# Performance work log

Measured on AMD Instinct MI355X. Metric: run time of the kernel, lower is better.

## Reference

```python
import jax, jax.numpy as jnp
import numpy as np
import math

NUM_HEAD = 16
D_MODEL = 1024
BATCH = 2
SEQ = 2048


def setup_inputs() -> dict:
    key = jax.random.key(0)
    k1, k2, k3, k4 = jax.random.split(key, 4)
    scale = 1.0 / math.sqrt(D_MODEL)
    return {
        "query": jax.random.normal(k1, (BATCH, SEQ, D_MODEL), dtype=jnp.float32),
        "key": jax.random.normal(k2, (BATCH, SEQ, D_MODEL), dtype=jnp.float32),
        "value": jax.random.normal(k3, (BATCH, SEQ, D_MODEL), dtype=jnp.float32),
        "w_concat": jax.random.normal(k4, (D_MODEL, D_MODEL), dtype=jnp.float32) * scale,
    }


def _split_heads(x):
    # [B, S, D] -> [B, H, S, d_k]
    B, S, D = x.shape
    return x.reshape(B, S, NUM_HEAD, D // NUM_HEAD).transpose(0, 2, 1, 3)


def reference(query, key, value, w_concat):
    # NOTE: faithful to the source bug — the w_q/w_k/w_v projections are
    # computed then discarded in the original forward; attention runs on the
    # raw (split) inputs.
    q = _split_heads(query)
    k = _split_heads(key)
    v = _split_heads(value)
    d_k = q.shape[-1]
    scores = jnp.einsum("bhqd,bhkd->bhqk", q, k) / math.sqrt(d_k)
    attn = jax.nn.softmax(scores, axis=-1)
    ctx = jnp.einsum("bhqk,bhkd->bhqd", attn, v)
    B, H, S, dk = ctx.shape
    x = ctx.transpose(0, 2, 1, 3).reshape(B, S, H * dk)
    # torch Linear (bias=False): y = x @ W^T
    return x @ w_concat.T
```

## Files before the change

### kernel.cpp

```cpp
#include <hip/hip_runtime.h>

#define BB 2
#define HH 16
#define SS 2048
#define DMODEL 1024

typedef unsigned short ushort_t;
typedef short bf16x8 __attribute__((ext_vector_type(8)));
typedef float f32x4 __attribute__((ext_vector_type(4)));

__device__ __forceinline__ unsigned short f2bf(float f) {
  union { float f; unsigned int u; } x; x.f = f;
  unsigned int u = x.u;
  return (unsigned short)((u + 0x7fffu + ((u >> 16) & 1u)) >> 16);
}
__device__ __forceinline__ unsigned int pack2(float a, float b) {
  return (unsigned int)f2bf(a) | ((unsigned int)f2bf(b) << 16);
}
__device__ __forceinline__ unsigned int cvtpk(float lo, float hi) {
  unsigned int r;
  asm("v_cvt_pk_bf16_f32 %0, %1, %2" : "=v"(r) : "v"(lo), "v"(hi));
  return r;
}
__device__ __forceinline__ void gload16(const ushort_t* g, ushort_t* l) {
  __builtin_amdgcn_global_load_lds(
      (const __attribute__((address_space(1))) void*)g,
      (__attribute__((address_space(3))) void*)l, 16, 0, 0);
}

__global__ void __launch_bounds__(256)
conv_qkv(const float* __restrict__ q, const float* __restrict__ k,
         const float* __restrict__ v, ushort_t* __restrict__ Qh,
         ushort_t* __restrict__ Kh, ushort_t* __restrict__ Vt) {
  const float c_sc = 0.18033688011112042f;
  __shared__ float vlds[64][65];
  int bh = blockIdx.y;
  int b = bh >> 4, h = bh & 15;
  int s0 = blockIdx.x * 64;
  int t = threadIdx.x;
#pragma unroll
  for (int j = 0; j < 4; ++j) {
    int idx = t + j * 256;
    int r = idx >> 4, c4 = idx & 15;
    size_t in_off = ((size_t)(b * SS + s0 + r)) * DMODEL + h * 64 + c4 * 4;
    float4 qa = *(const float4*)(q + in_off);
    float4 ka = *(const float4*)(k + in_off);
    float4 va = *(const float4*)(v + in_off);
    size_t out_off = ((size_t)bh * SS + s0 + r) * 64 + c4 * 4;
    *(uint2*)(Qh + out_off) = make_uint2(pack2(qa.x * c_sc, qa.y * c_sc),
                                         pack2(qa.z * c_sc, qa.w * c_sc));
    *(uint2*)(Kh + out_off) = make_uint2(pack2(ka.x, ka.y), pack2(ka.z, ka.w));
    vlds[r][c4 * 4 + 0] = va.x;
    vlds[r][c4 * 4 + 1] = va.y;
    vlds[r][c4 * 4 + 2] = va.z;
    vlds[r][c4 * 4 + 3] = va.w;
  }
  __syncthreads();
#pragma unroll
  for (int j = 0; j < 4; ++j) {
    int idx = t + j * 256;
    int d = idx >> 4, u = idx & 15;
    int c = ((u >> 3) << 1) | (u & 1);
    int g = (u >> 1) & 3;
    int m0 = c * 16 + g * 4;
    size_t voff = ((size_t)bh * 64 + d) * SS + s0 + u * 4;
    *(uint2*)(Vt + voff) =
        make_uint2(pack2(vlds[m0 + 0][d], vlds[m0 + 1][d]),
                   pack2(vlds[m0 + 2][d], vlds[m0 + 3][d]));
  }
}

__global__ void __launch_bounds__(256)
conv_w(const float* __restrict__ w, ushort_t* __restrict__ wb) {
  int i = blockIdx.x * 256 + threadIdx.x;
  float4 a = *(const float4*)(w + (size_t)i * 8);
  float4 b = *(const float4*)(w + (size_t)i * 8 + 4);
  uint4 o;
  o.x = pack2(a.x, a.y);
  o.y = pack2(a.z, a.w);
  o.z = pack2(b.x, b.y);
  o.w = pack2(b.z, b.w);
  *(uint4*)(wb + (size_t)i * 8) = o;
}

__global__ void __launch_bounds__(512, 1)
attn_fwd(const ushort_t* __restrict__ Qh, const ushort_t* __restrict__ Kh,
         const ushort_t* __restrict__ Vt, ushort_t* __restrict__ ctx) {
  __shared__ ushort_t K_lds[2][2][64][64];
  __shared__ ushort_t V_lds[2][2][64][64];
  __shared__ float cmb[4][64][21];
  int bh = blockIdx.y;
  int q0 = blockIdx.x * 256;
  int tid = threadIdx.x;
  int wid = tid >> 6;
  int half = wid >> 2;
  int wq = wid & 3;
  int lane = tid & 63;
  int g = lane >> 4, lr = lane & 15;
  int rsub = lane >> 3, ch = (lane & 7) ^ rsub;

  const ushort_t* Qp = Qh + (size_t)bh * SS * 64;
  const ushort_t* Kp = Kh + (size_t)bh * SS * 64;
  const ushort_t* Vp = Vt + (size_t)bh * 64 * SS;

  ushort_t (*Kl)[64][64] = K_lds[half];
  ushort_t (*Vl)[64][64] = V_lds[half];
  const int kvbase = half * (SS / 2);

  bf16x8 qf[4][2];
#pragma unroll
  for (int qb = 0; qb < 4; ++qb) {
    int row = q0 + wq * 64 + qb * 16 + lr;
#pragma unroll
    for (int kk = 0; kk < 2; ++kk)
      qf[qb][kk] = *(const bf16x8*)(Qp + (size_t)row * 64 + kk * 32 + g * 8);
  }

  const f32x4 vzero = {0.f, 0.f, 0.f, 0.f};
  const short ob = (short)0x3F80;
  const bf16x8 ones = {ob, ob, ob, ob, ob, ob, ob, ob};
  f32x4 o[4][4];
  f32x4 ol[4];
#pragma unroll
  for (int qb = 0; qb < 4; ++qb) {
    ol[qb] = vzero;
#pragma unroll
    for (int d = 0; d < 4; ++d) o[qb][d] = vzero;
  }

  auto stage = [&](int buf, int kv) {
#pragma unroll
    for (int j = 0; j < 2; ++j) {
      int i = j * 4 + wq;
      gload16(Kp + (size_t)(kv + i * 8 + rsub) * 64 + ch * 8, &Kl[buf][i * 8][0]);
      gload16(Vp + (size_t)(i * 8 + rsub) * SS + kv + ch * 8, &Vl[buf][i * 8][0]);
    }
  };

  const int NTH = SS / 128;
  auto tile = [&](int cur, int tl) {
    if (tl + 1 < NTH) stage(cur ^ 1, kvbase + (tl + 1) * 64);

    bf16x8 kf[4][2], vf[4][2];
#pragma unroll
    for (int c = 0; c < 4; ++c)
#pragma unroll
      for (int kk = 0; kk < 2; ++kk) {
        kf[c][kk] = *(const bf16x8*)&Kl[cur][c * 16 + lr]
                                       [((kk * 4 + g) ^ (lr & 7)) * 8];
        vf[c][kk] = *(const bf16x8*)&Vl[cur][c * 16 + lr]
                                       [((kk * 4 + g) ^ (lr & 7)) * 8];
      }

#pragma unroll
    for (int qb = 0; qb < 4; ++qb) {
      f32x4 s[4];
      __builtin_amdgcn_s_setprio(1);
#pragma unroll
      for (int c = 0; c < 4; ++c) {
        s[c] = __builtin_amdgcn_mfma_f32_16x16x32_bf16(kf[c][0], qf[qb][0], vzero, 0, 0, 0);
        s[c] = __builtin_amdgcn_mfma_f32_16x16x32_bf16(kf[c][1], qf[qb][1], s[c], 0, 0, 0);
      }
      __builtin_amdgcn_s_setprio(0);
      float p[4][4];
#pragma unroll
      for (int c = 0; c < 4; ++c)
#pragma unroll
        for (int r = 0; r < 4; ++r) p[c][r] = __builtin_amdgcn_exp2f(s[c][r]);
      bf16x8 pf[2];
#pragma unroll
      for (int kk = 0; kk < 2; ++kk) {
        uint4 w;
        w.x = cvtpk(p[kk * 2][0], p[kk * 2][1]);
        w.y = cvtpk(p[kk * 2][2], p[kk * 2][3]);
        w.z = cvtpk(p[kk * 2 + 1][0], p[kk * 2 + 1][1]);
        w.w = cvtpk(p[kk * 2 + 1][2], p[kk * 2 + 1][3]);
        pf[kk] = *(bf16x8*)&w;
      }
      __builtin_amdgcn_s_setprio(1);
      ol[qb] = __builtin_amdgcn_mfma_f32_16x16x32_bf16(pf[0], ones, ol[qb], 0, 0, 0);
      ol[qb] = __builtin_amdgcn_mfma_f32_16x16x32_bf16(pf[1], ones, ol[qb], 0, 0, 0);
#pragma unroll
      for (int d = 0; d < 4; ++d) {
        o[qb][d] = __builtin_amdgcn_mfma_f32_16x16x32_bf16(pf[0], vf[d][0], o[qb][d], 0, 0, 0);
        o[qb][d] = __builtin_amdgcn_mfma_f32_16x16x32_bf16(pf[1], vf[d][1], o[qb][d], 0, 0, 0);
      }
      __builtin_amdgcn_s_setprio(0);
    }
    __syncthreads();
  };

  stage(0, kvbase);
  __syncthreads();
#pragma unroll 1
  for (int tl = 0; tl < NTH; tl += 2) {
    tile(0, tl);
    tile(1, tl + 1);
  }

  int b = bh >> 4, h = bh & 15;
#pragma unroll
  for (int qb = 0; qb < 4; ++qb) {
    if (half) {
#pragma unroll
      for (int d = 0; d < 4; ++d)
#pragma unroll
        for (int r = 0; r < 4; ++r) cmb[wq][lane][d * 4 + r] = o[qb][d][r];
#pragma unroll
      for (int r = 0; r < 4; ++r) cmb[wq][lane][16 + r] = ol[qb][r];
    }
    __syncthreads();
    if (!half) {
      float linv[4];
#pragma unroll
      for (int r = 0; r < 4; ++r)
        linv[r] = __builtin_amdgcn_rcpf(ol[qb][r] + cmb[wq][lane][16 + r]);
#pragma unroll
      for (int d = 0; d < 4; ++d)
#pragma unroll
        for (int r = 0; r < 4; ++r) {
          float val = (o[qb][d][r] + cmb[wq][lane][d * 4 + r]) * linv[r];
          size_t row = (size_t)b * SS + q0 + wq * 64 + qb * 16 + g * 4 + r;
          ctx[row * DMODEL + h * 64 + d * 16 + lr] = f2bf(val);
        }
    }
    __syncthreads();
  }
}

__global__ void __launch_bounds__(256)
proj_gemm(const ushort_t* __restrict__ A, const ushort_t* __restrict__ Bw,
          float* __restrict__ out) {
  __shared__ ushort_t At[2][128][64];
  __shared__ ushort_t Bt[2][128][64];
  int m0 = blockIdx.x * 128, n0 = blockIdx.y * 128;
  int t = threadIdx.x;
  int wid = t >> 6, lane = t & 63;
  int wr = wid >> 1, wc = wid & 1;
  int g = lane >> 4, lr = lane & 15;
  int rsub = lane >> 3, ch = (lane & 7) ^ rsub;
  const f32x4 vzero = {0.f, 0.f, 0.f, 0.f};
  f32x4 acc[4][4];
#pragma unroll
  for (int m = 0; m < 4; ++m)
#pragma unroll
    for (int n = 0; n < 4; ++n) acc[m][n] = vzero;

  auto stage = [&](int buf, int k0) {
#pragma unroll
    for (int j = 0; j < 4; ++j) {
      int i = j * 4 + wid;
      gload16(A + (size_t)(m0 + i * 8 + rsub) * DMODEL + k0 + ch * 8, &At[buf][i * 8][0]);
      gload16(Bw + (size_t)(n0 + i * 8 + rsub) * DMODEL + k0 + ch * 8, &Bt[buf][i * 8][0]);
    }
  };

  const int NTK = DMODEL / 64;
  auto step = [&](int cur, int kt) {
    if (kt + 1 < NTK) stage(cur ^ 1, (kt + 1) * 64);
#pragma unroll
    for (int kk = 0; kk < 2; ++kk) {
      bf16x8 af[4], bf[4];
#pragma unroll
      for (int m = 0; m < 4; ++m)
        af[m] = *(const bf16x8*)&At[cur][wr * 64 + m * 16 + lr]
                                      [((kk * 4 + g) ^ (lr & 7)) * 8];
#pragma unroll
      for (int n = 0; n < 4; ++n)
        bf[n] = *(const bf16x8*)&Bt[cur][wc * 64 + n * 16 + lr]
                                      [((kk * 4 + g) ^ (lr & 7)) * 8];
#pragma unroll
      for (int m = 0; m < 4; ++m)
#pragma unroll
        for (int n = 0; n < 4; ++n)
          acc[m][n] = __builtin_amdgcn_mfma_f32_16x16x32_bf16(af[m], bf[n], acc[m][n], 0, 0, 0);
    }
    __syncthreads();
  };

  stage(0, 0);
  __syncthreads();
#pragma unroll 1
  for (int kt = 0; kt < NTK; kt += 2) {
    step(0, kt);
    step(1, kt + 1);
  }
#pragma unroll
  for (int m = 0; m < 4; ++m)
#pragma unroll
    for (int n = 0; n < 4; ++n)
#pragma unroll
      for (int r = 0; r < 4; ++r)
        out[(size_t)(m0 + wr * 64 + m * 16 + g * 4 + r) * DMODEL +
            n0 + wc * 64 + n * 16 + lr] = acc[m][n][r];
}

extern "C" void kernel_launch(void* const* d_in, const int* in_sizes, int n_in,
                              void* d_out, int out_size, void* d_ws, size_t ws_size,
                              hipStream_t stream) {
  const float* q = (const float*)d_in[0];
  const float* k = (const float*)d_in[1];
  const float* v = (const float*)d_in[2];
  const float* w = (const float*)d_in[3];
  float* out = (float*)d_out;

  size_t nqk = (size_t)BB * HH * SS * 64;
  ushort_t* Qh = (ushort_t*)d_ws;
  ushort_t* Kh = Qh + nqk;
  ushort_t* Vt = Kh + nqk;
  ushort_t* ctx = Vt + nqk;
  ushort_t* Wb = ctx + (size_t)BB * SS * DMODEL;
  size_t need = (4 * nqk + (size_t)DMODEL * DMODEL) * sizeof(ushort_t);
  if (ws_size < need) return;

  conv_qkv<<<dim3(SS / 64, BB * HH), 256, 0, stream>>>(q, k, v, Qh, Kh, Vt);
  conv_w<<<(DMODEL * DMODEL / 8) / 256, 256, 0, stream>>>(w, Wb);
  attn_fwd<<<dim3(SS / 256, BB * HH), 512, 0, stream>>>(Qh, Kh, Vt, ctx);
  proj_gemm<<<dim3((BB * SS) / 128, DMODEL / 128), 256, 0, stream>>>(ctx, Wb, out);
}
```

Baseline: 76.91 us.

## Fuse Q conversion into attention, batch combine stores, shrink projection GEMM tile

Q is no longer converted to a bf16 workspace buffer. The attention kernel loads fp32 Q directly and packs it to bf16 in registers, and the softmax scale is moved onto K in the conversion kernel. This removes one kernel's worth of Q write and read traffic. The cross-half combine in the epilogue now stores all four q-blocks at once with float4 writes and a single barrier instead of two barriers per q-block, at the cost of a larger LDS buffer. The projection GEMM tile is shrunk to 64x128 with launch bounds allowing 2 blocks per CU, giving more blocks and better occupancy, with less reuse per block.

After: 71.43 us. 7.1% less time.

```diff
diff --git a/kernel.cpp b/kernel.cpp
--- a/kernel.cpp
+++ b/kernel.cpp
@@ -29,9 +29,8 @@
 }
 
 __global__ void __launch_bounds__(256)
-conv_qkv(const float* __restrict__ q, const float* __restrict__ k,
-         const float* __restrict__ v, ushort_t* __restrict__ Qh,
-         ushort_t* __restrict__ Kh, ushort_t* __restrict__ Vt) {
+conv_kv(const float* __restrict__ k, const float* __restrict__ v,
+        ushort_t* __restrict__ Kh, ushort_t* __restrict__ Vt) {
   const float c_sc = 0.18033688011112042f;
   __shared__ float vlds[64][65];
   int bh = blockIdx.y;
@@ -43,13 +42,11 @@
     int idx = t + j * 256;
     int r = idx >> 4, c4 = idx & 15;
     size_t in_off = ((size_t)(b * SS + s0 + r)) * DMODEL + h * 64 + c4 * 4;
-    float4 qa = *(const float4*)(q + in_off);
     float4 ka = *(const float4*)(k + in_off);
     float4 va = *(const float4*)(v + in_off);
     size_t out_off = ((size_t)bh * SS + s0 + r) * 64 + c4 * 4;
-    *(uint2*)(Qh + out_off) = make_uint2(pack2(qa.x * c_sc, qa.y * c_sc),
-                                         pack2(qa.z * c_sc, qa.w * c_sc));
-    *(uint2*)(Kh + out_off) = make_uint2(pack2(ka.x, ka.y), pack2(ka.z, ka.w));
+    *(uint2*)(Kh + out_off) = make_uint2(pack2(ka.x * c_sc, ka.y * c_sc),
+                                         pack2(ka.z * c_sc, ka.w * c_sc));
     vlds[r][c4 * 4 + 0] = va.x;
     vlds[r][c4 * 4 + 1] = va.y;
     vlds[r][c4 * 4 + 2] = va.z;
@@ -84,12 +81,13 @@
 }
 
 __global__ void __launch_bounds__(512, 1)
-attn_fwd(const ushort_t* __restrict__ Qh, const ushort_t* __restrict__ Kh,
+attn_fwd(const float* __restrict__ Qsrc, const ushort_t* __restrict__ Kh,
          const ushort_t* __restrict__ Vt, ushort_t* __restrict__ ctx) {
   __shared__ ushort_t K_lds[2][2][64][64];
   __shared__ ushort_t V_lds[2][2][64][64];
-  __shared__ float cmb[4][64][21];
+  __shared__ __align__(16) float cmb[4][64][84];
   int bh = blockIdx.y;
+  int b = bh >> 4, h = bh & 15;
   int q0 = blockIdx.x * 256;
   int tid = threadIdx.x;
   int wid = tid >> 6;
@@ -99,7 +97,6 @@
   int g = lane >> 4, lr = lane & 15;
   int rsub = lane >> 3, ch = (lane & 7) ^ rsub;
 
-  const ushort_t* Qp = Qh + (size_t)bh * SS * 64;
   const ushort_t* Kp = Kh + (size_t)bh * SS * 64;
   const ushort_t* Vp = Vt + (size_t)bh * 64 * SS;
 
@@ -111,9 +108,18 @@
 #pragma unroll
   for (int qb = 0; qb < 4; ++qb) {
     int row = q0 + wq * 64 + qb * 16 + lr;
-#pragma unroll
-    for (int kk = 0; kk < 2; ++kk)
-      qf[qb][kk] = *(const bf16x8*)(Qp + (size_t)row * 64 + kk * 32 + g * 8);
+    const float* qr = Qsrc + ((size_t)(b * SS + row)) * DMODEL + h * 64;
+#pragma unroll
+    for (int kk = 0; kk < 2; ++kk) {
+      float4 x = *(const float4*)(qr + kk * 32 + g * 8);
+      float4 y = *(const float4*)(qr + kk * 32 + g * 8 + 4);
+      uint4 wv;
+      wv.x = cvtpk(x.x, x.y);
+      wv.y = cvtpk(x.z, x.w);
+      wv.z = cvtpk(y.x, y.y);
+      wv.w = cvtpk(y.z, y.w);
+      qf[qb][kk] = *(bf16x8*)&wv;
+    }
   }
 
   const f32x4 vzero = {0.f, 0.f, 0.f, 0.f};
@@ -198,59 +204,67 @@
     tile(1, tl + 1);
   }
 
-  int b = bh >> 4, h = bh & 15;
-#pragma unroll
-  for (int qb = 0; qb < 4; ++qb) {
-    if (half) {
+  if (half) {
+#pragma unroll
+    for (int qb = 0; qb < 4; ++qb) {
 #pragma unroll
       for (int d = 0; d < 4; ++d)
-#pragma unroll
-        for (int r = 0; r < 4; ++r) cmb[wq][lane][d * 4 + r] = o[qb][d][r];
-#pragma unroll
-      for (int r = 0; r < 4; ++r) cmb[wq][lane][16 + r] = ol[qb][r];
-    }
-    __syncthreads();
-    if (!half) {
+        *(float4*)&cmb[wq][lane][qb * 20 + d * 4] = *(float4*)&o[qb][d];
+      *(float4*)&cmb[wq][lane][qb * 20 + 16] = *(float4*)&ol[qb];
+    }
+  }
+  __syncthreads();
+  if (!half) {
+#pragma unroll
+    for (int qb = 0; qb < 4; ++qb) {
+      float4 lo = *(float4*)&cmb[wq][lane][qb * 20 + 16];
       float linv[4];
-#pragma unroll
-      for (int r = 0; r < 4; ++r)
-        linv[r] = __builtin_amdgcn_rcpf(ol[qb][r] + cmb[wq][lane][16 + r]);
-#pragma unroll
-      for (int d = 0; d < 4; ++d)
+      linv[0] = __builtin_amdgcn_rcpf(ol[qb][0] + lo.x);
+      linv[1] = __builtin_amdgcn_rcpf(ol[qb][1] + lo.y);
+      linv[2] = __builtin_amdgcn_rcpf(ol[qb][2] + lo.z);
+      linv[3] = __builtin_amdgcn_rcpf(ol[qb][3] + lo.w);
+#pragma unroll
+      for (int d = 0; d < 4; ++d) {
+        float4 oo = *(float4*)&cmb[wq][lane][qb * 20 + d * 4];
 #pragma unroll
         for (int r = 0; r < 4; ++r) {
-          float val = (o[qb][d][r] + cmb[wq][lane][d * 4 + r]) * linv[r];
+          float other = (r == 0) ? oo.x : (r == 1) ? oo.y : (r == 2) ? oo.z : oo.w;
+          float val = (o[qb][d][r] + other) * linv[r];
           size_t row = (size_t)b * SS + q0 + wq * 64 + qb * 16 + g * 4 + r;
           ctx[row * DMODEL + h * 64 + d * 16 + lr] = f2bf(val);
         }
-    }
-    __syncthreads();
-  }
-}
-
-__global__ void __launch_bounds__(256)
+      }
+    }
+  }
+}
+
+__global__ void __launch_bounds__(256, 2)
 proj_gemm(const ushort_t* __restrict__ A, const ushort_t* __restrict__ Bw,
           float* __restrict__ out) {
-  __shared__ ushort_t At[2][128][64];
+  __shared__ ushort_t At[2][64][64];
   __shared__ ushort_t Bt[2][128][64];
-  int m0 = blockIdx.x * 128, n0 = blockIdx.y * 128;
+  int m0 = blockIdx.x * 64, n0 = blockIdx.y * 128;
   int t = threadIdx.x;
   int wid = t >> 6, lane = t & 63;
   int wr = wid >> 1, wc = wid & 1;
   int g = lane >> 4, lr = lane & 15;
   int rsub = lane >> 3, ch = (lane & 7) ^ rsub;
   const f32x4 vzero = {0.f, 0.f, 0.f, 0.f};
-  f32x4 acc[4][4];
-#pragma unroll
-  for (int m = 0; m < 4; ++m)
+  f32x4 acc[2][4];
+#pragma unroll
+  for (int m = 0; m < 2; ++m)
 #pragma unroll
     for (int n = 0; n < 4; ++n) acc[m][n] = vzero;
 
   auto stage = [&](int buf, int k0) {
+#pragma unroll
+    for (int j = 0; j < 2; ++j) {
+      int i = j * 4 + wid;
+      gload16(A + (size_t)(m0 + i * 8 + rsub) * DMODEL + k0 + ch * 8, &At[buf][i * 8][0]);
+    }
 #pragma unroll
     for (int j = 0; j < 4; ++j) {
       int i = j * 4 + wid;
-      gload16(A + (size_t)(m0 + i * 8 + rsub) * DMODEL + k0 + ch * 8, &At[buf][i * 8][0]);
       gload16(Bw + (size_t)(n0 + i * 8 + rsub) * DMODEL + k0 + ch * 8, &Bt[buf][i * 8][0]);
     }
   };
@@ -260,17 +274,17 @@
     if (kt + 1 < NTK) stage(cur ^ 1, (kt + 1) * 64);
 #pragma unroll
     for (int kk = 0; kk < 2; ++kk) {
-      bf16x8 af[4], bf[4];
-#pragma unroll
-      for (int m = 0; m < 4; ++m)
-        af[m] = *(const bf16x8*)&At[cur][wr * 64 + m * 16 + lr]
+      bf16x8 af[2], bf[4];
+#pragma unroll
+      for (int m = 0; m < 2; ++m)
+        af[m] = *(const bf16x8*)&At[cur][wr * 32 + m * 16 + lr]
                                       [((kk * 4 + g) ^ (lr & 7)) * 8];
 #pragma unroll
       for (int n = 0; n < 4; ++n)
         bf[n] = *(const bf16x8*)&Bt[cur][wc * 64 + n * 16 + lr]
                                       [((kk * 4 + g) ^ (lr & 7)) * 8];
 #pragma unroll
-      for (int m = 0; m < 4; ++m)
+      for (int m = 0; m < 2; ++m)
 #pragma unroll
         for (int n = 0; n < 4; ++n)
           acc[m][n] = __builtin_amdgcn_mfma_f32_16x16x32_bf16(af[m], bf[n], acc[m][n], 0, 0, 0);
@@ -286,12 +300,12 @@
     step(1, kt + 1);
   }
 #pragma unroll
-  for (int m = 0; m < 4; ++m)
+  for (int m = 0; m < 2; ++m)
 #pragma unroll
     for (int n = 0; n < 4; ++n)
 #pragma unroll
       for (int r = 0; r < 4; ++r)
-        out[(size_t)(m0 + wr * 64 + m * 16 + g * 4 + r) * DMODEL +
+        out[(size_t)(m0 + wr * 32 + m * 16 + g * 4 + r) * DMODEL +
             n0 + wc * 64 + n * 16 + lr] = acc[m][n][r];
 }
 
@@ -305,16 +319,15 @@
   float* out = (float*)d_out;
 
   size_t nqk = (size_t)BB * HH * SS * 64;
-  ushort_t* Qh = (ushort_t*)d_ws;
-  ushort_t* Kh = Qh + nqk;
+  ushort_t* Kh = (ushort_t*)d_ws;
   ushort_t* Vt = Kh + nqk;
   ushort_t* ctx = Vt + nqk;
   ushort_t* Wb = ctx + (size_t)BB * SS * DMODEL;
-  size_t need = (4 * nqk + (size_t)DMODEL * DMODEL) * sizeof(ushort_t);
+  size_t need = (3 * nqk + (size_t)DMODEL * DMODEL) * sizeof(ushort_t);
   if (ws_size < need) return;
 
-  conv_qkv<<<dim3(SS / 64, BB * HH), 256, 0, stream>>>(q, k, v, Qh, Kh, Vt);
+  conv_kv<<<dim3(SS / 64, BB * HH), 256, 0, stream>>>(k, v, Kh, Vt);
   conv_w<<<(DMODEL * DMODEL / 8) / 256, 256, 0, stream>>>(w, Wb);
-  attn_fwd<<<dim3(SS / 256, BB * HH), 512, 0, stream>>>(Qh, Kh, Vt, ctx);
-  proj_gemm<<<dim3((BB * SS) / 128, DMODEL / 128), 256, 0, stream>>>(ctx, Wb, out);
-}
+  attn_fwd<<<dim3(SS / 256, BB * HH), 512, 0, stream>>>(q, Kh, Vt, ctx);
+  proj_gemm<<<dim3((BB * SS) / 64, DMODEL / 128), 256, 0, stream>>>(ctx, Wb, out);
+}
```
